# Kernel optimization log

Measured on AMD Instinct MI355X. Metric: run time of the kernel, lower is better.

## Reference

```python
import jax, jax.numpy as jnp
import numpy as np

D_MODEL = 1024
N_HEADS = 16
D_HEAD = D_MODEL // N_HEADS
B, T = 4, 2048


def setup_inputs() -> dict:
    key = jax.random.key(0)
    k1, k2, k3 = jax.random.split(key, 3)
    x = jax.random.normal(k1, (B, T, D_MODEL), dtype=jnp.float32)
    # nn.Linear(d_model, 3*d_model, bias=False): y = x @ W_qkv (stored here as [d, 3d])
    W_qkv = jax.random.normal(k2, (D_MODEL, 3 * D_MODEL), dtype=jnp.float32) * (D_MODEL ** -0.5)
    W_out = jax.random.normal(k3, (D_MODEL, D_MODEL), dtype=jnp.float32) * (D_MODEL ** -0.5)
    # causal mask: 1 = keep, 0 = masked (masked_fill(mask == 0, -inf))
    mask = jnp.tril(jnp.ones((T, T), dtype=jnp.int32))
    return {"x": x, "W_qkv": W_qkv, "W_out": W_out, "mask": mask}


def reference(x, W_qkv, W_out, mask):
    Bb, Tt, C = x.shape
    qkv = (x @ W_qkv).reshape(Bb, Tt, 3, N_HEADS, D_HEAD)
    q, k, v = qkv[:, :, 0], qkv[:, :, 1], qkv[:, :, 2]  # each [B,T,H,Dh]
    # scores: [B,H,T,T]
    attn = jnp.einsum('bthd,bshd->bhts', q, k) / jnp.sqrt(jnp.float32(D_HEAD))
    attn = jnp.where(mask == 0, -jnp.inf, attn)
    attn = jax.nn.softmax(attn, axis=-1)
    out = jnp.einsum('bhts,bshd->bthd', attn, v).reshape(Bb, Tt, C)
    return out @ W_out
```

## Files before the change

### kernel.cpp

```cpp
#include <hip/hip_runtime.h>
#include <cstdint>
#include <cstddef>


#define D_MODEL 1024
#define NHEADS  16
#define DHEAD   64
#define BATCH   4
#define SEQ     2048

typedef __attribute__((ext_vector_type(8))) _Float16 half8;
typedef __attribute__((ext_vector_type(4))) _Float16 half4;
typedef __attribute__((ext_vector_type(4))) float    f32x4;

__device__ __forceinline__ void async_copy16(const _Float16* g, _Float16* l) {
    __builtin_amdgcn_global_load_lds(
        (const __attribute__((address_space(1))) uint32_t*)g,
        (__attribute__((address_space(3))) uint32_t*)l, 16, 0, 0);
}

__global__ void cast_f32_f16(const float* __restrict__ in,
                             _Float16* __restrict__ out) {
    int i = blockIdx.x * blockDim.x + threadIdx.x;
    float4 v = *(const float4*)(in + (size_t)i * 4);
    half4 o;
    o.x = (_Float16)v.x; o.y = (_Float16)v.y;
    o.z = (_Float16)v.z; o.w = (_Float16)v.w;
    *(half4*)(out + (size_t)i * 4) = o;
}

__global__ void transpose_cast(const float* __restrict__ in,
                               _Float16* __restrict__ out, int R, int C) {
    __shared__ float tile[32][33];
    int c0 = blockIdx.x * 32, r0 = blockIdx.y * 32;
    int tx = threadIdx.x, ty = threadIdx.y;
    #pragma unroll
    for (int i = 0; i < 32; i += 8)
        tile[ty + i][tx] = in[(size_t)(r0 + ty + i) * C + c0 + tx];
    __syncthreads();
    #pragma unroll
    for (int i = 0; i < 32; i += 8)
        out[(size_t)(c0 + ty + i) * R + r0 + tx] = (_Float16)tile[tx][ty + i];
}

__global__ void gemm_qkv(const _Float16* __restrict__ A,
                         const _Float16* __restrict__ Bt,
                         _Float16* __restrict__ QK,
                         _Float16* __restrict__ Vtg) {
    __shared__ __attribute__((aligned(16))) _Float16 smem[128 * 132];
    _Float16* As = smem;
    _Float16* Bs = smem + 128 * 32;

    const int tid  = threadIdx.x;
    const int w    = tid >> 6, lane = tid & 63;
    const int l15  = lane & 15, quad = lane >> 4;
    const int wm   = w >> 1, wn = w & 1;
    const int row0 = blockIdx.y * 128, col0 = blockIdx.x * 128;
    const int K = 1024;

    f32x4 acc[4][4];
    #pragma unroll
    for (int i = 0; i < 4; i++)
        #pragma unroll
        for (int j = 0; j < 4; j++)
            acc[i][j] = (f32x4){0.f, 0.f, 0.f, 0.f};

    const int r0i = tid >> 2, c0i = tid & 3;
    const int r1i = (256 + tid) >> 2;

    for (int k0 = 0; k0 < K; k0 += 32) {
        __syncthreads();
        async_copy16(A  + (size_t)(row0 + r0i) * K + k0 + c0i * 8, &As[(w * 64) * 8]);
        async_copy16(A  + (size_t)(row0 + r1i) * K + k0 + c0i * 8, &As[(256 + w * 64) * 8]);
        async_copy16(Bt + (size_t)(col0 + r0i) * K + k0 + c0i * 8, &Bs[(w * 64) * 8]);
        async_copy16(Bt + (size_t)(col0 + r1i) * K + k0 + c0i * 8, &Bs[(256 + w * 64) * 8]);
        __syncthreads();

        half8 af[4], bfm[4];
        #pragma unroll
        for (int i = 0; i < 4; i++)
            af[i] = *(const half8*)&As[(wm * 64 + i * 16 + l15) * 32 + quad * 8];
        #pragma unroll
        for (int j = 0; j < 4; j++)
            bfm[j] = *(const half8*)&Bs[(wn * 64 + j * 16 + l15) * 32 + quad * 8];
        #pragma unroll
        for (int i = 0; i < 4; i++)
            #pragma unroll
            for (int j = 0; j < 4; j++)
                acc[i][j] = __builtin_amdgcn_mfma_f32_16x16x32_f16(
                    af[i], bfm[j], acc[i][j], 0, 0, 0);
    }

    if (blockIdx.x < 16) {
        #pragma unroll
        for (int i = 0; i < 4; i++) {
            int row = row0 + wm * 64 + i * 16 + quad * 4;
            #pragma unroll
            for (int j = 0; j < 4; j++) {
                int col = col0 + wn * 64 + j * 16 + l15;
                #pragma unroll
                for (int r = 0; r < 4; r++)
                    QK[(size_t)(row + r) * 2048 + col] = (_Float16)acc[i][j][r];
            }
        }
    } else {
        __syncthreads();
        #pragma unroll
        for (int i = 0; i < 4; i++) {
            int tl = wm * 64 + i * 16 + quad * 4;
            #pragma unroll
            for (int j = 0; j < 4; j++) {
                int vl = wn * 64 + j * 16 + l15;
                half4 pk;
                #pragma unroll
                for (int r = 0; r < 4; r++) pk[r] = (_Float16)acc[i][j][r];
                *(half4*)&smem[vl * 132 + tl] = pk;
            }
        }
        __syncthreads();
        const int bb = row0 >> 11, tb = row0 & 2047;
        const int rr0 = tid >> 4;
        const int cc  = (tid & 15) * 8;
        #pragma unroll
        for (int s = 0; s < 8; s++) {
            int vl = rr0 + s * 16;
            int vcol = (col0 - 2048) + vl;
            int hh = vcol >> 6, d = vcol & 63;
            *(half8*)&Vtg[((size_t)((bb * 16 + hh) * 64 + d)) * 2048 + tb + cc] =
                *(const half8*)&smem[vl * 132 + cc];
        }
    }
}

__global__ void gemm_out(const _Float16* __restrict__ A,
                         const _Float16* __restrict__ Bt,
                         float* __restrict__ Cf, int N, int K) {
    __shared__ __attribute__((aligned(16))) _Float16 As[128 * 32];
    __shared__ __attribute__((aligned(16))) _Float16 Bs[128 * 32];

    const int tid  = threadIdx.x;
    const int w    = tid >> 6, lane = tid & 63;
    const int l15  = lane & 15, quad = lane >> 4;
    const int wm   = w >> 1, wn = w & 1;
    const int row0 = blockIdx.y * 128, col0 = blockIdx.x * 128;

    f32x4 acc[4][4];
    #pragma unroll
    for (int i = 0; i < 4; i++)
        #pragma unroll
        for (int j = 0; j < 4; j++)
            acc[i][j] = (f32x4){0.f, 0.f, 0.f, 0.f};

    const int r0i = tid >> 2, c0i = tid & 3;
    const int r1i = (256 + tid) >> 2;

    for (int k0 = 0; k0 < K; k0 += 32) {
        __syncthreads();
        async_copy16(A  + (size_t)(row0 + r0i) * K + k0 + c0i * 8, &As[(w * 64) * 8]);
        async_copy16(A  + (size_t)(row0 + r1i) * K + k0 + c0i * 8, &As[(256 + w * 64) * 8]);
        async_copy16(Bt + (size_t)(col0 + r0i) * K + k0 + c0i * 8, &Bs[(w * 64) * 8]);
        async_copy16(Bt + (size_t)(col0 + r1i) * K + k0 + c0i * 8, &Bs[(256 + w * 64) * 8]);
        __syncthreads();

        half8 af[4], bfm[4];
        #pragma unroll
        for (int i = 0; i < 4; i++)
            af[i] = *(const half8*)&As[(wm * 64 + i * 16 + l15) * 32 + quad * 8];
        #pragma unroll
        for (int j = 0; j < 4; j++)
            bfm[j] = *(const half8*)&Bs[(wn * 64 + j * 16 + l15) * 32 + quad * 8];
        #pragma unroll
        for (int i = 0; i < 4; i++)
            #pragma unroll
            for (int j = 0; j < 4; j++)
                acc[i][j] = __builtin_amdgcn_mfma_f32_16x16x32_f16(
                    af[i], bfm[j], acc[i][j], 0, 0, 0);
    }

    #pragma unroll
    for (int i = 0; i < 4; i++) {
        int row = row0 + wm * 64 + i * 16 + quad * 4;
        #pragma unroll
        for (int j = 0; j < 4; j++) {
            int col = col0 + wn * 64 + j * 16 + l15;
            #pragma unroll
            for (int r = 0; r < 4; r++)
                Cf[(size_t)(row + r) * N + col] = acc[i][j][r];
        }
    }
}

#define PREFETCH(t)                                                          \
    do {                                                                     \
        const _Float16* kp_ = kb + (size_t)((t) * 64 + srow) * 2048 + sc;    \
        kr0 = *(const half8*)kp_;                                            \
        kr1 = *(const half8*)(kp_ + (size_t)32 * 2048);                      \
        const _Float16* vp_ = vb + (size_t)srow * 2048 + (t) * 64 + sc;      \
        vr0 = *(const half8*)vp_;                                            \
        vr1 = *(const half8*)(vp_ + (size_t)32 * 2048);                      \
    } while (0)

__global__ __launch_bounds__(256, 2) void flash_attn(
        const _Float16* __restrict__ qk, const _Float16* __restrict__ vt,
        _Float16* __restrict__ obuf) {
    const int pr = blockIdx.x, h = blockIdx.y, b = blockIdx.z;
    const int tid = threadIdx.x;
    const int w = tid >> 6, lane = tid & 63;
    const int l15 = lane & 15, quad = lane >> 4;

    __shared__ __attribute__((aligned(16))) _Float16 Ks[64 * 72];
    __shared__ __attribute__((aligned(16))) _Float16 Vs[64 * 72];
    __shared__ __attribute__((aligned(16))) _Float16 Pl[4][32 * 72];

    const _Float16* kb = qk + (size_t)b * SEQ * 2048 + D_MODEL + h * 64;
    const _Float16* vb = vt + (size_t)(b * 16 + h) * 64 * 2048;

    const int srow = tid >> 3;
    const int sc   = (tid & 7) * 8;

    const _Float16 QSCL = (_Float16)0.18033688f;

    #pragma unroll 1
    for (int phase = 0; phase < 2; ++phase) {
        const int tq = phase ? (15 - pr) : pr;
        const int q0 = tq * 128;
        const int n_iter = 2 * (tq + 1);

        half8 qf[2][2];
        #pragma unroll
        for (int g = 0; g < 2; g++) {
            const _Float16* qp = qk
                + ((size_t)(b * SEQ + q0 + w * 32 + g * 16 + l15)) * 2048
                + h * DHEAD + quad * 8;
            qf[g][0] = *(const half8*)qp;
            qf[g][1] = *(const half8*)(qp + 32);
            #pragma unroll
            for (int j = 0; j < 8; j++) {
                qf[g][0][j] *= QSCL;
                qf[g][1][j] *= QSCL;
            }
        }

        f32x4 o[2][4];
        float l_acc[2] = {0.f, 0.f};
        #pragma unroll
        for (int g = 0; g < 2; g++)
            #pragma unroll
            for (int d = 0; d < 4; d++) o[g][d] = (f32x4){0.f, 0.f, 0.f, 0.f};

        half8 kr0, kr1, vr0, vr1;
        PREFETCH(0);

        #pragma unroll 1
        for (int it = 0; it < n_iter; ++it) {
            __syncthreads();
            *(half8*)&Ks[srow * 72 + sc]        = kr0;
            *(half8*)&Ks[(srow + 32) * 72 + sc] = kr1;
            *(half8*)&Vs[srow * 72 + sc]        = vr0;
            *(half8*)&Vs[(srow + 32) * 72 + sc] = vr1;
            __syncthreads();

            if (it + 1 < n_iter) PREFETCH(it + 1);

            f32x4 st[2][4];
            __builtin_amdgcn_s_setprio(1);
            #pragma unroll
            for (int nt = 0; nt < 4; nt++) {
                half8 ka0 = *(const half8*)&Ks[(nt * 16 + l15) * 72 + quad * 8];
                half8 ka1 = *(const half8*)&Ks[(nt * 16 + l15) * 72 + 32 + quad * 8];
                #pragma unroll
                for (int g = 0; g < 2; g++) {
                    f32x4 acc = (f32x4){0.f, 0.f, 0.f, 0.f};
                    acc = __builtin_amdgcn_mfma_f32_16x16x32_f16(ka0, qf[g][0], acc, 0, 0, 0);
                    acc = __builtin_amdgcn_mfma_f32_16x16x32_f16(ka1, qf[g][1], acc, 0, 0, 0);
                    st[g][nt] = acc;
                }
            }
            __builtin_amdgcn_s_setprio(0);

            #pragma unroll
            for (int g = 0; g < 2; g++) {
                const int c0 = __builtin_amdgcn_readfirstlane(
                    q0 + w * 32 + g * 16 - 64 * it);
                if (c0 < 63) {
                    #pragma unroll
                    for (int nt = 0; nt < 4; nt++)
                        #pragma unroll
                        for (int r = 0; r < 4; r++)
                            if (nt * 16 + quad * 4 + r - l15 > c0)
                                st[g][nt][r] = -INFINITY;
                }
                #pragma unroll
                for (int nt = 0; nt < 4; nt++) {
                    float p0 = exp2f(st[g][nt][0]);
                    float p1 = exp2f(st[g][nt][1]);
                    float p2 = exp2f(st[g][nt][2]);
                    float p3 = exp2f(st[g][nt][3]);
                    l_acc[g] += (p0 + p1) + (p2 + p3);
                    auto lo = __builtin_amdgcn_cvt_pkrtz(p0, p1);
                    auto hi = __builtin_amdgcn_cvt_pkrtz(p2, p3);
                    half4 pk;
                    pk[0] = (_Float16)lo[0]; pk[1] = (_Float16)lo[1];
                    pk[2] = (_Float16)hi[0]; pk[3] = (_Float16)hi[1];
                    *(half4*)&Pl[w][(g * 16 + l15) * 72 + nt * 16 + quad * 4] = pk;
                }
            }
            asm volatile("s_waitcnt lgkmcnt(0)" ::: "memory");

            __builtin_amdgcn_s_setprio(1);
            #pragma unroll
            for (int kf = 0; kf < 2; kf++) {
                half8 pf0 = *(const half8*)&Pl[w][l15 * 72 + kf * 32 + quad * 8];
                half8 pf1 = *(const half8*)&Pl[w][(16 + l15) * 72 + kf * 32 + quad * 8];
                #pragma unroll
                for (int dt = 0; dt < 4; dt++) {
                    half8 vf = *(const half8*)&Vs[(dt * 16 + l15) * 72 + kf * 32 + quad * 8];
                    o[0][dt] = __builtin_amdgcn_mfma_f32_16x16x32_f16(pf0, vf, o[0][dt], 0, 0, 0);
                    o[1][dt] = __builtin_amdgcn_mfma_f32_16x16x32_f16(pf1, vf, o[1][dt], 0, 0, 0);
                }
            }
            __builtin_amdgcn_s_setprio(0);
        }

        #pragma unroll
        for (int g = 0; g < 2; g++) {
            float l = l_acc[g];
            l += __shfl_xor(l, 16);
            l += __shfl_xor(l, 32);
            float linv[4];
            #pragma unroll
            for (int r = 0; r < 4; r++)
                linv[r] = 1.0f / __shfl(l, quad * 4 + r, 16);

            _Float16* ob = obuf
                + ((size_t)(b * SEQ + q0 + w * 32 + g * 16 + quad * 4)) * D_MODEL
                + h * DHEAD;
            #pragma unroll
            for (int r = 0; r < 4; r++) {
                #pragma unroll
                for (int dt = 0; dt < 4; dt++)
                    ob[(size_t)r * D_MODEL + dt * 16 + l15] =
                        (_Float16)(o[g][dt][r] * linv[r]);
            }
        }
        __syncthreads();
    }
}

extern "C" void kernel_launch(void* const* d_in, const int* in_sizes, int n_in,
                              void* d_out, int out_size, void* d_ws, size_t ws_size,
                              hipStream_t stream) {
    const float* x    = (const float*)d_in[0];
    const float* Wqkv = (const float*)d_in[1];
    const float* Wout = (const float*)d_in[2];
    float* out = (float*)d_out;

    char* ws = (char*)d_ws;
    _Float16* Xh   = (_Float16*)(ws);
    _Float16* WqT  = (_Float16*)(ws + ((size_t)16 << 20));
    _Float16* WoT  = (_Float16*)(ws + ((size_t)23 << 20));
    _Float16* QKb  = (_Float16*)(ws + ((size_t)26 << 20));
    _Float16* Vtg  = (_Float16*)(ws + ((size_t)58 << 20));
    _Float16* Obuf = (_Float16*)(ws + ((size_t)74 << 20));

    cast_f32_f16<<<8192, 256, 0, stream>>>(x, Xh);
    transpose_cast<<<dim3(96, 32), dim3(32, 8), 0, stream>>>(Wqkv, WqT, 1024, 3072);
    transpose_cast<<<dim3(32, 32), dim3(32, 8), 0, stream>>>(Wout, WoT, 1024, 1024);
    gemm_qkv<<<dim3(24, 64), 256, 0, stream>>>(Xh, WqT, QKb, Vtg);
    flash_attn<<<dim3(8, NHEADS, BATCH), 256, 0, stream>>>(QKb, Vtg, Obuf);
    gemm_out<<<dim3(8, 64), 256, 0, stream>>>(Obuf, WoT, out, 1024, 1024);
}
```

Measured before the change: 271.2 us.

## Split flash-attention query tile across 8 waves of 16 rows each

```diff
diff --git a/kernel.cpp b/kernel.cpp
--- a/kernel.cpp
+++ b/kernel.cpp
@@ -192,15 +192,11 @@
 
 #define PREFETCH(t)                                                          \
     do {                                                                     \
-        const _Float16* kp_ = kb + (size_t)((t) * 64 + srow) * 2048 + sc;    \
-        kr0 = *(const half8*)kp_;                                            \
-        kr1 = *(const half8*)(kp_ + (size_t)32 * 2048);                      \
-        const _Float16* vp_ = vb + (size_t)srow * 2048 + (t) * 64 + sc;      \
-        vr0 = *(const half8*)vp_;                                            \
-        vr1 = *(const half8*)(vp_ + (size_t)32 * 2048);                      \
+        kr0 = *(const half8*)(kb + (size_t)((t) * 64 + srow) * 2048 + sc);   \
+        vr0 = *(const half8*)(vb + (size_t)srow * 2048 + (t) * 64 + sc);     \
     } while (0)
 
-__global__ __launch_bounds__(256, 2) void flash_attn(
+__global__ __launch_bounds__(512, 4) void flash_attn(
         const _Float16* __restrict__ qk, const _Float16* __restrict__ vt,
         _Float16* __restrict__ obuf) {
     const int pr = blockIdx.x, h = blockIdx.y, b = blockIdx.z;
@@ -210,7 +206,7 @@
 
     __shared__ __attribute__((aligned(16))) _Float16 Ks[64 * 72];
     __shared__ __attribute__((aligned(16))) _Float16 Vs[64 * 72];
-    __shared__ __attribute__((aligned(16))) _Float16 Pl[4][32 * 72];
+    __shared__ __attribute__((aligned(16))) _Float16 Pl[8][16 * 72];
 
     const _Float16* kb = qk + (size_t)b * SEQ * 2048 + D_MODEL + h * 64;
     const _Float16* vb = vt + (size_t)(b * 16 + h) * 64 * 2048;
@@ -226,83 +222,74 @@
         const int q0 = tq * 128;
         const int n_iter = 2 * (tq + 1);
 
-        half8 qf[2][2];
-        #pragma unroll
-        for (int g = 0; g < 2; g++) {
+        half8 qf[2];
+        {
             const _Float16* qp = qk
-                + ((size_t)(b * SEQ + q0 + w * 32 + g * 16 + l15)) * 2048
+                + ((size_t)(b * SEQ + q0 + w * 16 + l15)) * 2048
                 + h * DHEAD + quad * 8;
-            qf[g][0] = *(const half8*)qp;
-            qf[g][1] = *(const half8*)(qp + 32);
+            qf[0] = *(const half8*)qp;
+            qf[1] = *(const half8*)(qp + 32);
             #pragma unroll
             for (int j = 0; j < 8; j++) {
-                qf[g][0][j] *= QSCL;
-                qf[g][1][j] *= QSCL;
-            }
-        }
-
-        f32x4 o[2][4];
-        float l_acc[2] = {0.f, 0.f};
-        #pragma unroll
-        for (int g = 0; g < 2; g++)
-            #pragma unroll
-            for (int d = 0; d < 4; d++) o[g][d] = (f32x4){0.f, 0.f, 0.f, 0.f};
-
-        half8 kr0, kr1, vr0, vr1;
+                qf[0][j] *= QSCL;
+                qf[1][j] *= QSCL;
+            }
+        }
+
+        f32x4 o[4];
+        float l_acc = 0.f;
+        #pragma unroll
+        for (int d = 0; d < 4; d++) o[d] = (f32x4){0.f, 0.f, 0.f, 0.f};
+
+        half8 kr0, vr0;
         PREFETCH(0);
 
         #pragma unroll 1
         for (int it = 0; it < n_iter; ++it) {
             __syncthreads();
-            *(half8*)&Ks[srow * 72 + sc]        = kr0;
-            *(half8*)&Ks[(srow + 32) * 72 + sc] = kr1;
-            *(half8*)&Vs[srow * 72 + sc]        = vr0;
-            *(half8*)&Vs[(srow + 32) * 72 + sc] = vr1;
+            *(half8*)&Ks[srow * 72 + sc] = kr0;
+            *(half8*)&Vs[srow * 72 + sc] = vr0;
             __syncthreads();
 
             if (it + 1 < n_iter) PREFETCH(it + 1);
 
-            f32x4 st[2][4];
+            f32x4 st[4];
             __builtin_amdgcn_s_setprio(1);
             #pragma unroll
             for (int nt = 0; nt < 4; nt++) {
                 half8 ka0 = *(const half8*)&Ks[(nt * 16 + l15) * 72 + quad * 8];
                 half8 ka1 = *(const half8*)&Ks[(nt * 16 + l15) * 72 + 32 + quad * 8];
-                #pragma unroll
-                for (int g = 0; g < 2; g++) {
-                    f32x4 acc = (f32x4){0.f, 0.f, 0.f, 0.f};
-                    acc = __builtin_amdgcn_mfma_f32_16x16x32_f16(ka0, qf[g][0], acc, 0, 0, 0);
-                    acc = __builtin_amdgcn_mfma_f32_16x16x32_f16(ka1, qf[g][1], acc, 0, 0, 0);
-                    st[g][nt] = acc;
-                }
+                f32x4 acc = (f32x4){0.f, 0.f, 0.f, 0.f};
+                acc = __builtin_amdgcn_mfma_f32_16x16x32_f16(ka0, qf[0], acc, 0, 0, 0);
+                acc = __builtin_amdgcn_mfma_f32_16x16x32_f16(ka1, qf[1], acc, 0, 0, 0);
+                st[nt] = acc;
             }
             __builtin_amdgcn_s_setprio(0);
 
-            #pragma unroll
-            for (int g = 0; g < 2; g++) {
+            {
                 const int c0 = __builtin_amdgcn_readfirstlane(
-                    q0 + w * 32 + g * 16 - 64 * it);
+                    q0 + w * 16 - 64 * it);
                 if (c0 < 63) {
                     #pragma unroll
                     for (int nt = 0; nt < 4; nt++)
                         #pragma unroll
                         for (int r = 0; r < 4; r++)
                             if (nt * 16 + quad * 4 + r - l15 > c0)
-                                st[g][nt][r] = -INFINITY;
+                                st[nt][r] = -INFINITY;
                 }
                 #pragma unroll
                 for (int nt = 0; nt < 4; nt++) {
-                    float p0 = exp2f(st[g][nt][0]);
-                    float p1 = exp2f(st[g][nt][1]);
-                    float p2 = exp2f(st[g][nt][2]);
-                    float p3 = exp2f(st[g][nt][3]);
-                    l_acc[g] += (p0 + p1) + (p2 + p3);
+                    float p0 = exp2f(st[nt][0]);
+                    float p1 = exp2f(st[nt][1]);
+                    float p2 = exp2f(st[nt][2]);
+                    float p3 = exp2f(st[nt][3]);
+                    l_acc += (p0 + p1) + (p2 + p3);
                     auto lo = __builtin_amdgcn_cvt_pkrtz(p0, p1);
                     auto hi = __builtin_amdgcn_cvt_pkrtz(p2, p3);
                     half4 pk;
                     pk[0] = (_Float16)lo[0]; pk[1] = (_Float16)lo[1];
                     pk[2] = (_Float16)hi[0]; pk[3] = (_Float16)hi[1];
-                    *(half4*)&Pl[w][(g * 16 + l15) * 72 + nt * 16 + quad * 4] = pk;
+                    *(half4*)&Pl[w][l15 * 72 + nt * 16 + quad * 4] = pk;
                 }
             }
             asm volatile("s_waitcnt lgkmcnt(0)" ::: "memory");
@@ -310,21 +297,18 @@
             __builtin_amdgcn_s_setprio(1);
             #pragma unroll
             for (int kf = 0; kf < 2; kf++) {
-                half8 pf0 = *(const half8*)&Pl[w][l15 * 72 + kf * 32 + quad * 8];
-                half8 pf1 = *(const half8*)&Pl[w][(16 + l15) * 72 + kf * 32 + quad * 8];
+                half8 pf = *(const half8*)&Pl[w][l15 * 72 + kf * 32 + quad * 8];
                 #pragma unroll
                 for (int dt = 0; dt < 4; dt++) {
                     half8 vf = *(const half8*)&Vs[(dt * 16 + l15) * 72 + kf * 32 + quad * 8];
-                    o[0][dt] = __builtin_amdgcn_mfma_f32_16x16x32_f16(pf0, vf, o[0][dt], 0, 0, 0);
-                    o[1][dt] = __builtin_amdgcn_mfma_f32_16x16x32_f16(pf1, vf, o[1][dt], 0, 0, 0);
+                    o[dt] = __builtin_amdgcn_mfma_f32_16x16x32_f16(pf, vf, o[dt], 0, 0, 0);
                 }
             }
             __builtin_amdgcn_s_setprio(0);
         }
 
-        #pragma unroll
-        for (int g = 0; g < 2; g++) {
-            float l = l_acc[g];
+        {
+            float l = l_acc;
             l += __shfl_xor(l, 16);
             l += __shfl_xor(l, 32);
             float linv[4];
@@ -333,14 +317,14 @@
                 linv[r] = 1.0f / __shfl(l, quad * 4 + r, 16);
 
             _Float16* ob = obuf
-                + ((size_t)(b * SEQ + q0 + w * 32 + g * 16 + quad * 4)) * D_MODEL
+                + ((size_t)(b * SEQ + q0 + w * 16 + quad * 4)) * D_MODEL
                 + h * DHEAD;
             #pragma unroll
             for (int r = 0; r < 4; r++) {
                 #pragma unroll
                 for (int dt = 0; dt < 4; dt++)
                     ob[(size_t)r * D_MODEL + dt * 16 + l15] =
-                        (_Float16)(o[g][dt][r] * linv[r]);
+                        (_Float16)(o[dt][r] * linv[r]);
             }
         }
         __syncthreads();
@@ -367,6 +351,6 @@
     transpose_cast<<<dim3(96, 32), dim3(32, 8), 0, stream>>>(Wqkv, WqT, 1024, 3072);
     transpose_cast<<<dim3(32, 32), dim3(32, 8), 0, stream>>>(Wout, WoT, 1024, 1024);
     gemm_qkv<<<dim3(24, 64), 256, 0, stream>>>(Xh, WqT, QKb, Vtg);
-    flash_attn<<<dim3(8, NHEADS, BATCH), 256, 0, stream>>>(QKb, Vtg, Obuf);
+    flash_attn<<<dim3(8, NHEADS, BATCH), 512, 0, stream>>>(QKb, Vtg, Obuf);
     gemm_out<<<dim3(8, 64), 256, 0, stream>>>(Obuf, WoT, out, 1024, 1024);
 }
```

Measured after the change: 272.0 us. Within noise of the previous version (+0.3%).

## Double flash-attention KV tile to 128 keys and use native exp2

Applied to the files above, without the earlier changes.

```diff
diff --git a/kernel.cpp b/kernel.cpp
--- a/kernel.cpp
+++ b/kernel.cpp
@@ -17,6 +17,14 @@
     __builtin_amdgcn_global_load_lds(
         (const __attribute__((address_space(1))) uint32_t*)g,
         (__attribute__((address_space(3))) uint32_t*)l, 16, 0, 0);
+}
+
+__device__ __forceinline__ float fast_exp2(float x) {
+#if __has_builtin(__builtin_amdgcn_exp2f)
+    return __builtin_amdgcn_exp2f(x);
+#else
+    return exp2f(x);
+#endif
 }
 
 __global__ void cast_f32_f16(const float* __restrict__ in,
@@ -192,12 +200,16 @@
 
 #define PREFETCH(t)                                                          \
     do {                                                                     \
-        const _Float16* kp_ = kb + (size_t)((t) * 64 + srow) * 2048 + sc;    \
+        const _Float16* kp_ = kb + (size_t)((t) * 128 + srow) * 2048 + sc;   \
         kr0 = *(const half8*)kp_;                                            \
         kr1 = *(const half8*)(kp_ + (size_t)32 * 2048);                      \
-        const _Float16* vp_ = vb + (size_t)srow * 2048 + (t) * 64 + sc;      \
+        kr2 = *(const half8*)(kp_ + (size_t)64 * 2048);                      \
+        kr3 = *(const half8*)(kp_ + (size_t)96 * 2048);                      \
+        const _Float16* vp_ = vb + (size_t)srow * 2048 + (t) * 128 + sc;     \
         vr0 = *(const half8*)vp_;                                            \
-        vr1 = *(const half8*)(vp_ + (size_t)32 * 2048);                      \
+        vr1 = *(const half8*)(vp_ + 64);                                     \
+        vr2 = *(const half8*)(vp_ + (size_t)32 * 2048);                      \
+        vr3 = *(const half8*)(vp_ + (size_t)32 * 2048 + 64);                 \
     } while (0)
 
 __global__ __launch_bounds__(256, 2) void flash_attn(
@@ -208,9 +220,9 @@
     const int w = tid >> 6, lane = tid & 63;
     const int l15 = lane & 15, quad = lane >> 4;
 
-    __shared__ __attribute__((aligned(16))) _Float16 Ks[64 * 72];
-    __shared__ __attribute__((aligned(16))) _Float16 Vs[64 * 72];
-    __shared__ __attribute__((aligned(16))) _Float16 Pl[4][32 * 72];
+    __shared__ __attribute__((aligned(16))) _Float16 Ks[128 * 72];
+    __shared__ __attribute__((aligned(16))) _Float16 Vs[64 * 136];
+    __shared__ __attribute__((aligned(16))) _Float16 Pl[4][32 * 136];
 
     const _Float16* kb = qk + (size_t)b * SEQ * 2048 + D_MODEL + h * 64;
     const _Float16* vb = vt + (size_t)(b * 16 + h) * 64 * 2048;
@@ -224,7 +236,7 @@
     for (int phase = 0; phase < 2; ++phase) {
         const int tq = phase ? (15 - pr) : pr;
         const int q0 = tq * 128;
-        const int n_iter = 2 * (tq + 1);
+        const int n_iter = tq + 1;
 
         half8 qf[2][2];
         #pragma unroll
@@ -248,73 +260,82 @@
             #pragma unroll
             for (int d = 0; d < 4; d++) o[g][d] = (f32x4){0.f, 0.f, 0.f, 0.f};
 
-        half8 kr0, kr1, vr0, vr1;
+        half8 kr0, kr1, kr2, kr3, vr0, vr1, vr2, vr3;
         PREFETCH(0);
 
         #pragma unroll 1
         for (int it = 0; it < n_iter; ++it) {
             __syncthreads();
-            *(half8*)&Ks[srow * 72 + sc]        = kr0;
-            *(half8*)&Ks[(srow + 32) * 72 + sc] = kr1;
-            *(half8*)&Vs[srow * 72 + sc]        = vr0;
-            *(half8*)&Vs[(srow + 32) * 72 + sc] = vr1;
+            *(half8*)&Ks[(srow      ) * 72 + sc] = kr0;
+            *(half8*)&Ks[(srow + 32 ) * 72 + sc] = kr1;
+            *(half8*)&Ks[(srow + 64 ) * 72 + sc] = kr2;
+            *(half8*)&Ks[(srow + 96 ) * 72 + sc] = kr3;
+            *(half8*)&Vs[srow * 136 + sc]             = vr0;
+            *(half8*)&Vs[srow * 136 + sc + 64]        = vr1;
+            *(half8*)&Vs[(srow + 32) * 136 + sc]      = vr2;
+            *(half8*)&Vs[(srow + 32) * 136 + sc + 64] = vr3;
             __syncthreads();
 
             if (it + 1 < n_iter) PREFETCH(it + 1);
 
-            f32x4 st[2][4];
+            #pragma unroll
+            for (int hh = 0; hh < 2; hh++) {
+                f32x4 st[2][4];
+                __builtin_amdgcn_s_setprio(1);
+                #pragma unroll
+                for (int n4 = 0; n4 < 4; n4++) {
+                    const int nt = hh * 4 + n4;
+                    half8 ka0 = *(const half8*)&Ks[(nt * 16 + l15) * 72 + quad * 8];
+                    half8 ka1 = *(const half8*)&Ks[(nt * 16 + l15) * 72 + 32 + quad * 8];
+                    #pragma unroll
+                    for (int g = 0; g < 2; g++) {
+                        f32x4 acc = (f32x4){0.f, 0.f, 0.f, 0.f};
+                        acc = __builtin_amdgcn_mfma_f32_16x16x32_f16(ka0, qf[g][0], acc, 0, 0, 0);
+                        acc = __builtin_amdgcn_mfma_f32_16x16x32_f16(ka1, qf[g][1], acc, 0, 0, 0);
+                        st[g][n4] = acc;
+                    }
+                }
+                __builtin_amdgcn_s_setprio(0);
+
+                #pragma unroll
+                for (int g = 0; g < 2; g++) {
+                    const int c0 = __builtin_amdgcn_readfirstlane(
+                        q0 + w * 32 + g * 16 - 128 * it);
+                    if (c0 < 127) {
+                        #pragma unroll
+                        for (int n4 = 0; n4 < 4; n4++)
+                            #pragma unroll
+                            for (int r = 0; r < 4; r++)
+                                if ((hh * 4 + n4) * 16 + quad * 4 + r - l15 > c0)
+                                    st[g][n4][r] = -INFINITY;
+                    }
+                    #pragma unroll
+                    for (int n4 = 0; n4 < 4; n4++) {
+                        const int nt = hh * 4 + n4;
+                        float p0 = fast_exp2(st[g][n4][0]);
+                        float p1 = fast_exp2(st[g][n4][1]);
+                        float p2 = fast_exp2(st[g][n4][2]);
+                        float p3 = fast_exp2(st[g][n4][3]);
+                        l_acc[g] += (p0 + p1) + (p2 + p3);
+                        auto lo = __builtin_amdgcn_cvt_pkrtz(p0, p1);
+                        auto hi = __builtin_amdgcn_cvt_pkrtz(p2, p3);
+                        half4 pk;
+                        pk[0] = (_Float16)lo[0]; pk[1] = (_Float16)lo[1];
+                        pk[2] = (_Float16)hi[0]; pk[3] = (_Float16)hi[1];
+                        *(half4*)&Pl[w][(g * 16 + l15) * 136 + nt * 16 + quad * 4] = pk;
+                    }
+                }
+            }
+            asm volatile("s_waitcnt lgkmcnt(0)" ::: "memory");
+
             __builtin_amdgcn_s_setprio(1);
             #pragma unroll
-            for (int nt = 0; nt < 4; nt++) {
-                half8 ka0 = *(const half8*)&Ks[(nt * 16 + l15) * 72 + quad * 8];
-                half8 ka1 = *(const half8*)&Ks[(nt * 16 + l15) * 72 + 32 + quad * 8];
-                #pragma unroll
-                for (int g = 0; g < 2; g++) {
-                    f32x4 acc = (f32x4){0.f, 0.f, 0.f, 0.f};
-                    acc = __builtin_amdgcn_mfma_f32_16x16x32_f16(ka0, qf[g][0], acc, 0, 0, 0);
-                    acc = __builtin_amdgcn_mfma_f32_16x16x32_f16(ka1, qf[g][1], acc, 0, 0, 0);
-                    st[g][nt] = acc;
-                }
-            }
-            __builtin_amdgcn_s_setprio(0);
-
-            #pragma unroll
-            for (int g = 0; g < 2; g++) {
-                const int c0 = __builtin_amdgcn_readfirstlane(
-                    q0 + w * 32 + g * 16 - 64 * it);
-                if (c0 < 63) {
-                    #pragma unroll
-                    for (int nt = 0; nt < 4; nt++)
-                        #pragma unroll
-                        for (int r = 0; r < 4; r++)
-                            if (nt * 16 + quad * 4 + r - l15 > c0)
-                                st[g][nt][r] = -INFINITY;
-                }
-                #pragma unroll
-                for (int nt = 0; nt < 4; nt++) {
-                    float p0 = exp2f(st[g][nt][0]);
-                    float p1 = exp2f(st[g][nt][1]);
-                    float p2 = exp2f(st[g][nt][2]);
-                    float p3 = exp2f(st[g][nt][3]);
-                    l_acc[g] += (p0 + p1) + (p2 + p3);
-                    auto lo = __builtin_amdgcn_cvt_pkrtz(p0, p1);
-                    auto hi = __builtin_amdgcn_cvt_pkrtz(p2, p3);
-                    half4 pk;
-                    pk[0] = (_Float16)lo[0]; pk[1] = (_Float16)lo[1];
-                    pk[2] = (_Float16)hi[0]; pk[3] = (_Float16)hi[1];
-                    *(half4*)&Pl[w][(g * 16 + l15) * 72 + nt * 16 + quad * 4] = pk;
-                }
-            }
-            asm volatile("s_waitcnt lgkmcnt(0)" ::: "memory");
-
-            __builtin_amdgcn_s_setprio(1);
-            #pragma unroll
-            for (int kf = 0; kf < 2; kf++) {
-                half8 pf0 = *(const half8*)&Pl[w][l15 * 72 + kf * 32 + quad * 8];
-                half8 pf1 = *(const half8*)&Pl[w][(16 + l15) * 72 + kf * 32 + quad * 8];
+            for (int kf = 0; kf < 4; kf++) {
+                half8 pf0 = *(const half8*)&Pl[w][l15 * 136 + kf * 32 + quad * 8];
+                half8 pf1 = *(const half8*)&Pl[w][(16 + l15) * 136 + kf * 32 + quad * 8];
                 #pragma unroll
                 for (int dt = 0; dt < 4; dt++) {
-                    half8 vf = *(const half8*)&Vs[(dt * 16 + l15) * 72 + kf * 32 + quad * 8];
+                    half8 vf = *(const half8*)&Vs[(dt * 16 + l15) * 136 + kf * 32 + quad * 8];
                     o[0][dt] = __builtin_amdgcn_mfma_f32_16x16x32_f16(pf0, vf, o[0][dt], 0, 0, 0);
                     o[1][dt] = __builtin_amdgcn_mfma_f32_16x16x32_f16(pf1, vf, o[1][dt], 0, 0, 0);
                 }
```

Result: faster. 263.2 us (-2.9%).
